# Performance work log

Measured on AMD Instinct MI355X. Metric: run time of the kernel, lower is better.

## Reference

```python
import jax, jax.numpy as jnp
import numpy as np

N_ACTIVE = 32

def setup_inputs() -> dict:
    key = jax.random.key(0)
    ks = jax.random.split(key, 6)
    B, T, D, G, GD = 4, 2048, 2048, 4096, 256
    x = jax.random.normal(ks[0], (B, T, D), jnp.float32)
    Wc = jax.random.normal(ks[1], (G, D), jnp.float32) * (D ** -0.5)   # context_proj weight
    temperature = jnp.array(1.0, jnp.float32)
    genes = jax.random.normal(ks[2], (G, GD), jnp.float32) * 0.02      # dna_bank gene table
    Wd = jax.random.normal(ks[3], (D, GD), jnp.float32) * (GD ** -0.5) # gene_to_down weight
    Wu = jax.random.normal(ks[4], (D, GD), jnp.float32) * 0.02         # gene_to_up (zeros in init; random for testing)
    norm_w = jnp.ones((D,), jnp.float32)                               # RMSNorm weight
    scale = jnp.array(0.1, jnp.float32)
    return {"x": x, "Wc": Wc, "temperature": temperature, "genes": genes,
            "Wd": Wd, "Wu": Wu, "norm_w": norm_w, "scale": scale}

def reference(x, Wc, temperature, genes, Wd, Wu, norm_w, scale):
    # RMSNorm (torch default eps = finfo(dtype).eps, learnable elementwise weight)
    eps = jnp.finfo(x.dtype).eps
    xn = x * jax.lax.rsqrt(jnp.mean(x * x, axis=-1, keepdims=True) + eps) * norm_w
    # Expression: router logits over gene bank, temperature clamped at 0.1
    logits = jnp.einsum('btd,gd->btg', xn, Wc) / jnp.clip(temperature, 0.1)
    # top-k + scatter(-inf) + softmax == softmax over top-k values, zeros elsewhere
    top_vals, top_idx = jax.lax.top_k(logits, N_ACTIVE)        # (B,T,K)
    expr_w = jax.nn.softmax(top_vals, axis=-1)                 # (B,T,K)
    # dna_bank.express: weighted combination of genes. Only top-k entries are
    # nonzero, so gather + weighted sum is mathematically identical to the
    # dense (B,T,G)@(G,GD) combine the original materializes.
    expressed = jnp.einsum('btk,btkc->btc', expr_w, genes[top_idx])  # (B,T,GD)
    down = jnp.tanh(jnp.einsum('btc,dc->btd', expressed, Wd))
    up = jnp.einsum('btc,dc->btd', expressed, Wu)
    return down * xn * up * scale
```

## Files before the change

kernel.cpp:

```cpp
#include <hip/hip_runtime.h>
#include <math.h>

#define M_TOK 8192
#define D_DIM 2048
#define G_GENES 4096
#define GD_DIM 256
#define KSEL 32
#define NCAND 40
#define NSLICE 8

typedef float f32x4 __attribute__((ext_vector_type(4)));
typedef short bf16x8 __attribute__((ext_vector_type(8)));

__device__ __forceinline__ void async_copy16(const void* g, void* lds) {
  __builtin_amdgcn_global_load_lds((const __attribute__((address_space(1))) void*)g,
                                   (__attribute__((address_space(3))) void*)lds, 16, 0, 0);
}

__device__ __forceinline__ unsigned short f2bf(float f) {
  unsigned int u = __float_as_uint(f);
  unsigned int r = (u + 0x7fffu + ((u >> 16) & 1u)) >> 16;
  return (unsigned short)r;
}
__device__ __forceinline__ float bf2f(unsigned short h) {
  return __uint_as_float(((unsigned int)h) << 16);
}

__global__ __launch_bounds__(256) void k1_rmsnorm(const float* __restrict__ x,
                                                  const float* __restrict__ nw,
                                                  float* __restrict__ r_out,
                                                  unsigned short* __restrict__ xn_bf) {
  int t = blockIdx.x, tid = threadIdx.x;
  const float4* xr = (const float4*)(x + (size_t)t * D_DIM);
  float4 a = xr[tid], b = xr[tid + 256];
  double ss = (double)a.x*a.x + (double)a.y*a.y + (double)a.z*a.z + (double)a.w*a.w
            + (double)b.x*b.x + (double)b.y*b.y + (double)b.z*b.z + (double)b.w*b.w;
  for (int off = 32; off; off >>= 1) ss += __shfl_down(ss, off);
  __shared__ double sred[4];
  __shared__ float rshare;
  int lane = tid & 63, wv = tid >> 6;
  if (lane == 0) sred[wv] = ss;
  __syncthreads();
  if (tid == 0) {
    double tot = sred[0] + sred[1] + sred[2] + sred[3];
    float r = (float)(1.0 / sqrt(tot / (double)D_DIM + 1.1920928955078125e-7));
    rshare = r; r_out[t] = r;
  }
  __syncthreads();
  float r = rshare;
  const float4* nw4 = (const float4*)nw;
  float4 na = nw4[tid], nb = nw4[tid + 256];
  ushort4 oa, ob;
  oa.x = f2bf(a.x * r * na.x); oa.y = f2bf(a.y * r * na.y);
  oa.z = f2bf(a.z * r * na.z); oa.w = f2bf(a.w * r * na.w);
  ob.x = f2bf(b.x * r * nb.x); ob.y = f2bf(b.y * r * nb.y);
  ob.z = f2bf(b.z * r * nb.z); ob.w = f2bf(b.w * r * nb.w);
  ushort4* o4 = (ushort4*)(xn_bf + (size_t)t * D_DIM);
  o4[tid] = oa; o4[tid + 256] = ob;
}

__global__ __launch_bounds__(256) void k2_cvt(const float* __restrict__ w,
                                              unsigned short* __restrict__ wb) {
  size_t i = (size_t)blockIdx.x * 256 + threadIdx.x;
  const float4* w4 = (const float4*)w;
  float4 a = w4[2*i], b = w4[2*i+1];
  ushort4 oa, ob;
  oa.x = f2bf(a.x); oa.y = f2bf(a.y); oa.z = f2bf(a.z); oa.w = f2bf(a.w);
  ob.x = f2bf(b.x); ob.y = f2bf(b.y); ob.z = f2bf(b.z); ob.w = f2bf(b.w);
  ((ushort4*)wb)[2*i] = oa; ((ushort4*)wb)[2*i+1] = ob;
}

__global__ __launch_bounds__(256) void k2b_split(const float* __restrict__ wd,
                                                 const float* __restrict__ wu,
                                                 unsigned short* __restrict__ wdh,
                                                 unsigned short* __restrict__ wdl,
                                                 unsigned short* __restrict__ wuh,
                                                 unsigned short* __restrict__ wul) {
  const float* src = blockIdx.y ? wu : wd;
  unsigned short* dh = blockIdx.y ? wuh : wdh;
  unsigned short* dl = blockIdx.y ? wul : wdl;
  size_t i = (size_t)blockIdx.x * 256 + threadIdx.x;
  float4 v = ((const float4*)src)[i];
  ushort4 h, l;
  h.x = f2bf(v.x); l.x = f2bf(v.x - bf2f(h.x));
  h.y = f2bf(v.y); l.y = f2bf(v.y - bf2f(h.y));
  h.z = f2bf(v.z); l.z = f2bf(v.z - bf2f(h.z));
  h.w = f2bf(v.w); l.w = f2bf(v.w - bf2f(h.w));
  ((ushort4*)dh)[i] = h;
  ((ushort4*)dl)[i] = l;
}

__global__ __launch_bounds__(512, 1) void k3_gemm_logits(const unsigned short* __restrict__ A,
                                                         const unsigned short* __restrict__ B,
                                                         unsigned short* __restrict__ C) {
  __shared__ unsigned short As[4][256 * 32];
  __shared__ unsigned short Bs[4][256 * 32];
  const int tid = threadIdx.x;
  const int lane = tid & 63, wv = tid >> 6;
  const int wm = wv >> 2, wn = wv & 3;
  int lin = blockIdx.x;
  int swz = (lin & 7) * 64 + (lin >> 3);
  const int bm = swz & 31, bn = swz >> 5;

  const int grow = lane >> 2;
  const int gslot = (lane & 3) ^ ((lane >> 3) & 3);
  const unsigned short* agp = A + (size_t)(bm * 256 + wv * 32 + grow) * D_DIM + gslot * 8;
  const unsigned short* bgp = B + (size_t)(bn * 256 + wv * 32 + grow) * D_DIM + gslot * 8;
  const int fr = lane & 15;
  const int sw8 = (((lane >> 4) ^ ((lane >> 1) & 3))) * 8;

  f32x4 acc[8][4];
#pragma unroll
  for (int m = 0; m < 8; ++m)
#pragma unroll
    for (int n = 0; n < 4; ++n) acc[m][n] = (f32x4){0.f, 0.f, 0.f, 0.f};

#define STAGE_A3(t_) { const int b_ = (t_) & 3; const int kt_ = (t_) * 32;          \
    async_copy16(agp + kt_,              &As[b_][(wv * 32) * 32]);                   \
    async_copy16(agp + kt_ + 16 * D_DIM, &As[b_][(wv * 32 + 16) * 32]); }
#define STAGE_B3(t_) { const int b_ = (t_) & 3; const int kt_ = (t_) * 32;          \
    async_copy16(bgp + kt_,              &Bs[b_][(wv * 32) * 32]);                   \
    async_copy16(bgp + kt_ + 16 * D_DIM, &Bs[b_][(wv * 32 + 16) * 32]); }

  STAGE_A3(0); STAGE_B3(0);
  STAGE_A3(1); STAGE_B3(1);
  STAGE_A3(2); STAGE_B3(2);
  asm volatile("s_waitcnt vmcnt(8)" ::: "memory");
  __builtin_amdgcn_s_barrier();

#pragma unroll 1
  for (int t = 0; t < 64; ++t) {
    const int c = t & 3;
    const unsigned short* as = As[c];
    const unsigned short* bs = Bs[c];
    bf16x8 fa[4], fb[4];
#pragma unroll
    for (int n = 0; n < 4; ++n)
      fb[n] = *(const bf16x8*)&bs[(wn * 64 + n * 16 + fr) * 32 + sw8];
#pragma unroll
    for (int m = 0; m < 4; ++m)
      fa[m] = *(const bf16x8*)&as[(wm * 128 + m * 16 + fr) * 32 + sw8];
    if (t + 3 < 64) STAGE_A3(t + 3);
    __builtin_amdgcn_s_barrier();
    asm volatile("s_waitcnt lgkmcnt(0)" ::: "memory");
    __builtin_amdgcn_sched_barrier(0);
    __builtin_amdgcn_s_setprio(1);
#pragma unroll
    for (int m = 0; m < 4; ++m)
#pragma unroll
      for (int n = 0; n < 4; ++n)
        acc[m][n] = __builtin_amdgcn_mfma_f32_16x16x32_bf16(fa[m], fb[n], acc[m][n], 0, 0, 0);
    __builtin_amdgcn_s_setprio(0);
    __builtin_amdgcn_s_barrier();
#pragma unroll
    for (int m = 0; m < 4; ++m)
      fa[m] = *(const bf16x8*)&as[(wm * 128 + 64 + m * 16 + fr) * 32 + sw8];
    if (t + 3 < 64) STAGE_B3(t + 3);
    __builtin_amdgcn_s_barrier();
    asm volatile("s_waitcnt lgkmcnt(0)" ::: "memory");
    __builtin_amdgcn_sched_barrier(0);
    __builtin_amdgcn_s_setprio(1);
#pragma unroll
    for (int m = 0; m < 4; ++m)
#pragma unroll
      for (int n = 0; n < 4; ++n)
        acc[m + 4][n] = __builtin_amdgcn_mfma_f32_16x16x32_bf16(fa[m], fb[n], acc[m + 4][n], 0, 0, 0);
    __builtin_amdgcn_s_setprio(0);
    if (t <= 60)      { asm volatile("s_waitcnt vmcnt(8)" ::: "memory"); }
    else if (t == 61) { asm volatile("s_waitcnt vmcnt(4)" ::: "memory"); }
    else if (t == 62) { asm volatile("s_waitcnt vmcnt(0)" ::: "memory"); }
    __builtin_amdgcn_s_barrier();
  }
#undef STAGE_A3
#undef STAGE_B3

#pragma unroll
  for (int m = 0; m < 8; ++m)
#pragma unroll
    for (int n = 0; n < 4; ++n)
#pragma unroll
      for (int j = 0; j < 4; ++j) {
        int row = bm * 256 + wm * 128 + m * 16 + (lane >> 4) * 4 + j;
        int col = bn * 256 + wn * 64 + n * 16 + fr;
        C[(size_t)row * G_GENES + col] = f2bf(acc[m][n][j]);
      }
}

__global__ __launch_bounds__(256) void k4_topk(const unsigned short* __restrict__ L,
                                               int* __restrict__ cand) {
  int wv = threadIdx.x >> 6, lane = threadIdx.x & 63;
  int t = blockIdx.x * 4 + wv;
  const unsigned short* lp = L + (size_t)t * G_GENES;
  unsigned kp[32];
#pragma unroll
  for (int i = 0; i < 8; ++i) {
    uint4 raw = *(const uint4*)(lp + i * 512 + lane * 8);
    unsigned rr[4] = {raw.x, raw.y, raw.z, raw.w};
#pragma unroll
    for (int q = 0; q < 4; ++q) {
      unsigned r = rr[q];
      unsigned s = (r >> 15) & 0x00010001u;
      unsigned xm = 0x80008000u | (s * 0x7FFFu);
      kp[i * 4 + q] = r ^ xm;
    }
  }
  unsigned lo = 0, hi = 65536;
  while (hi - lo > 1u) {
    unsigned mid = (lo + hi) >> 1;
    int c = 0;
#pragma unroll
    for (int q = 0; q < 32; ++q) {
      c += __popcll(__ballot((kp[q] & 0xFFFFu) >= mid));
      c += __popcll(__ballot((kp[q] >> 16) >= mid));
    }
    if (c >= NCAND) lo = mid; else hi = mid;
  }
  const unsigned T = lo;
  unsigned long long below = (1ull << lane) - 1ull;
  int* outp = cand + (size_t)t * NCAND;
  int cnt = 0;
#pragma unroll
  for (int q = 0; q < 32; ++q) {
#pragma unroll
    for (int h = 0; h < 2; ++h) {
      unsigned key = h ? (kp[q] >> 16) : (kp[q] & 0xFFFFu);
      bool pred = key > T;
      unsigned long long m = __ballot(pred);
      if (pred) {
        int pos = cnt + (int)__popcll(m & below);
        outp[pos] = (q >> 2) * 512 + lane * 8 + (q & 3) * 2 + h;
      }
      cnt += (int)__popcll(m);
    }
  }
#pragma unroll 1
  for (int q = 0; q < 32 && cnt < NCAND; ++q) {
#pragma unroll
    for (int h = 0; h < 2; ++h) {
      unsigned key = h ? (kp[q] >> 16) : (kp[q] & 0xFFFFu);
      bool pred = key == T;
      unsigned long long m = __ballot(pred);
      if (pred) {
        int pos = cnt + (int)__popcll(m & below);
        if (pos < NCAND)
          outp[pos] = (q >> 2) * 512 + lane * 8 + (q & 3) * 2 + h;
      }
      cnt += (int)__popcll(m);
    }
  }
}

__global__ __launch_bounds__(256) void k5a_partial(const float* __restrict__ x,
                                                   const float* __restrict__ r,
                                                   const float* __restrict__ nw,
                                                   const float* __restrict__ Wc,
                                                   const int* __restrict__ cand,
                                                   double* __restrict__ part) {
  int bid = blockIdx.x;
  int slice = bid & 7;
  int group = bid >> 3;
  int wv = threadIdx.x >> 6, lane = threadIdx.x & 63;
  const int dbase = slice * 256;
  float4 nv = *(const float4*)(nw + dbase + lane * 4);
  bool b0 = (lane & 1) != 0, b1 = (lane & 2) != 0, b2 = (lane & 4) != 0;
#pragma unroll 1
  for (int tt = 0; tt < 2; ++tt) {
    int t = group * 8 + wv * 2 + tt;
    float rr = r[t];
    float4 xv = *(const float4*)(x + (size_t)t * D_DIM + dbase + lane * 4);
    float4 xl;
    xl.x = xv.x * rr * nv.x;
    xl.y = xv.y * rr * nv.y;
    xl.z = xv.z * rr * nv.z;
    xl.w = xv.w * rr * nv.w;
    int myg = cand[t * NCAND + (lane < NCAND ? lane : 0)];
    double* outp = part + ((size_t)t * NSLICE + slice) * NCAND;
#pragma unroll 1
    for (int j0 = 0; j0 < NCAND; j0 += 8) {
      float4 w[8];
#pragma unroll
      for (int c = 0; c < 8; ++c) {
        int g = __shfl(myg, j0 + c);
        w[c] = *(const float4*)(Wc + (size_t)g * D_DIM + dbase + lane * 4);
      }
      double s[8];
#pragma unroll
      for (int c = 0; c < 8; ++c)
        s[c] = ((double)xl.x * (double)w[c].x + (double)xl.y * (double)w[c].y)
             + ((double)xl.z * (double)w[c].z + (double)xl.w * (double)w[c].w);
      double u01 = b0 ? s[1] : s[0], t01 = b0 ? s[0] : s[1];
      double u23 = b0 ? s[3] : s[2], t23 = b0 ? s[2] : s[3];
      double u45 = b0 ? s[5] : s[4], t45 = b0 ? s[4] : s[5];
      double u67 = b0 ? s[7] : s[6], t67 = b0 ? s[6] : s[7];
      u01 += __shfl_xor(t01, 1);
      u23 += __shfl_xor(t23, 1);
      u45 += __shfl_xor(t45, 1);
      u67 += __shfl_xor(t67, 1);
      double v03 = b1 ? u23 : u01, t03 = b1 ? u01 : u23;
      double v47 = b1 ? u67 : u45, t47 = b1 ? u45 : u67;
      v03 += __shfl_xor(t03, 2);
      v47 += __shfl_xor(t47, 2);
      double wsum = b2 ? v47 : v03, t07 = b2 ? v03 : v47;
      wsum += __shfl_xor(t07, 4);
      wsum += __shfl_xor(wsum, 8);
      wsum += __shfl_xor(wsum, 16);
      wsum += __shfl_xor(wsum, 32);
      if (lane < 8) outp[j0 + lane] = wsum;
    }
  }
}

__global__ __launch_bounds__(256) void k6_express(const double* __restrict__ part,
                                                  const int* __restrict__ cand,
                                                  const float* __restrict__ genes,
                                                  const float* __restrict__ temp,
                                                  unsigned short* __restrict__ e_hi,
                                                  unsigned short* __restrict__ e_lo) {
  int t = blockIdx.x, tid = threadIdx.x;
  __shared__ double sval[NCAND];
  __shared__ int sidx[NCAND];
  __shared__ float sw[NCAND];
  float tclamp = fmaxf(temp[0], 0.1f);
  if (tid < NCAND) {
    const double* pp = part + (size_t)t * NSLICE * NCAND + tid;
    double v = 0.0;
#pragma unroll
    for (int s = 0; s < NSLICE; ++s) v += pp[s * NCAND];
    sval[tid] = v / (double)tclamp;
    sidx[tid] = cand[(size_t)t * NCAND + tid];
  }
  __syncthreads();
  if (tid < 64) {
    double v = (tid < NCAND) ? sval[tid] : -1.0e300;
    int gi = (tid < NCAND) ? sidx[tid] : 0x7fffffff;
    int rank = 0;
    for (int j = 0; j < NCAND; ++j) {
      double vj = sval[j]; int gj = sidx[j];
      if (vj > v || (vj == v && gj < gi)) rank++;
    }
    bool sel = (tid < NCAND) && (rank < KSEL);
    double vs = sel ? v : -1.0e300;
    double mx = vs;
    for (int off = 32; off; off >>= 1) { double o = __shfl_xor(mx, off); mx = fmax(mx, o); }
    double e = sel ? exp(v - mx) : 0.0;
    double ssum = e;
    for (int off = 32; off; off >>= 1) ssum += __shfl_xor(ssum, off);
    if (tid < NCAND) sw[tid] = (float)(e / ssum);
  }
  __syncthreads();
  float a0 = 0.f, a1 = 0.f, a2 = 0.f, a3 = 0.f;
#pragma unroll
  for (int k = 0; k < NCAND; k += 4) {
    a0 += sw[k]     * genes[(size_t)sidx[k]     * GD_DIM + tid];
    a1 += sw[k + 1] * genes[(size_t)sidx[k + 1] * GD_DIM + tid];
    a2 += sw[k + 2] * genes[(size_t)sidx[k + 2] * GD_DIM + tid];
    a3 += sw[k + 3] * genes[(size_t)sidx[k + 3] * GD_DIM + tid];
  }
  float acc = (a0 + a1) + (a2 + a3);
  unsigned short h = f2bf(acc);
  unsigned short l = f2bf(acc - bf2f(h));
  e_hi[(size_t)t * GD_DIM + tid] = h;
  e_lo[(size_t)t * GD_DIM + tid] = l;
}

__global__ __launch_bounds__(256) void k7_mfma(const unsigned short* __restrict__ e_hi,
                                               const unsigned short* __restrict__ e_lo,
                                               const unsigned short* __restrict__ wdh,
                                               const unsigned short* __restrict__ wdl,
                                               const unsigned short* __restrict__ wuh,
                                               const unsigned short* __restrict__ wul,
                                               const float* __restrict__ x,
                                               const float* __restrict__ r,
                                               const float* __restrict__ nw,
                                               const float* __restrict__ scale_p,
                                               float* __restrict__ out) {
  __shared__ unsigned short Ah[128 * 32], Al[128 * 32];
  __shared__ unsigned short Dh[64 * 32], Dl[64 * 32], Uh[64 * 32], Ul[64 * 32];
  int tid = threadIdx.x;
  int lane = tid & 63, wv = tid >> 6;
  int bn = blockIdx.x, bm = blockIdx.y;
  int wr = wv >> 1, wc = wv & 1;
  const int lrow = lane >> 2;
  const int lcol = (lane & 3) * 8;

  f32x4 accD[4][2], accU[4][2];
#pragma unroll
  for (int m = 0; m < 4; ++m)
#pragma unroll
    for (int n = 0; n < 2; ++n) {
      accD[m][n] = (f32x4){0.f, 0.f, 0.f, 0.f};
      accU[m][n] = (f32x4){0.f, 0.f, 0.f, 0.f};
    }

  for (int kt = 0; kt < GD_DIM; kt += 32) {
    __syncthreads();
#pragma unroll
    for (int c = 0; c < 8; ++c) {
      int cid = wv * 8 + c;
      if (cid < 8) {
        async_copy16(e_hi + (size_t)(bm * 128 + cid * 16 + lrow) * GD_DIM + kt + lcol,
                     &Ah[cid * 512]);
      } else if (cid < 16) {
        int cc = cid - 8;
        async_copy16(e_lo + (size_t)(bm * 128 + cc * 16 + lrow) * GD_DIM + kt + lcol,
                     &Al[cc * 512]);
      } else if (cid < 20) {
        int cc = cid - 16;
        async_copy16(wdh + (size_t)(bn * 64 + cc * 16 + lrow) * GD_DIM + kt + lcol,
                     &Dh[cc * 512]);
      } else if (cid < 24) {
        int cc = cid - 20;
        async_copy16(wdl + (size_t)(bn * 64 + cc * 16 + lrow) * GD_DIM + kt + lcol,
                     &Dl[cc * 512]);
      } else if (cid < 28) {
        int cc = cid - 24;
        async_copy16(wuh + (size_t)(bn * 64 + cc * 16 + lrow) * GD_DIM + kt + lcol,
                     &Uh[cc * 512]);
      } else {
        int cc = cid - 28;
        async_copy16(wul + (size_t)(bn * 64 + cc * 16 + lrow) * GD_DIM + kt + lcol,
                     &Ul[cc * 512]);
      }
    }
    __syncthreads();
    bf16x8 fah[4], fal[4], fdh[2], fdl[2], fuh[2], ful[2];
#pragma unroll
    for (int m = 0; m < 4; ++m) {
      int off = (wr * 64 + m * 16 + (lane & 15)) * 32 + (lane >> 4) * 8;
      fah[m] = *(const bf16x8*)&Ah[off];
      fal[m] = *(const bf16x8*)&Al[off];
    }
#pragma unroll
    for (int n = 0; n < 2; ++n) {
      int off = (wc * 32 + n * 16 + (lane & 15)) * 32 + (lane >> 4) * 8;
      fdh[n] = *(const bf16x8*)&Dh[off];
      fdl[n] = *(const bf16x8*)&Dl[off];
      fuh[n] = *(const bf16x8*)&Uh[off];
      ful[n] = *(const bf16x8*)&Ul[off];
    }
#pragma unroll
    for (int m = 0; m < 4; ++m)
#pragma unroll
      for (int n = 0; n < 2; ++n) {
        accD[m][n] = __builtin_amdgcn_mfma_f32_16x16x32_bf16(fah[m], fdh[n], accD[m][n], 0, 0, 0);
        accD[m][n] = __builtin_amdgcn_mfma_f32_16x16x32_bf16(fah[m], fdl[n], accD[m][n], 0, 0, 0);
        accD[m][n] = __builtin_amdgcn_mfma_f32_16x16x32_bf16(fal[m], fdh[n], accD[m][n], 0, 0, 0);
        accU[m][n] = __builtin_amdgcn_mfma_f32_16x16x32_bf16(fah[m], fuh[n], accU[m][n], 0, 0, 0);
        accU[m][n] = __builtin_amdgcn_mfma_f32_16x16x32_bf16(fah[m], ful[n], accU[m][n], 0, 0, 0);
        accU[m][n] = __builtin_amdgcn_mfma_f32_16x16x32_bf16(fal[m], fuh[n], accU[m][n], 0, 0, 0);
      }
  }
  float sc = scale_p[0];
#pragma unroll
  for (int m = 0; m < 4; ++m)
#pragma unroll
    for (int j = 0; j < 4; ++j) {
      int token = bm * 128 + wr * 64 + m * 16 + (lane >> 4) * 4 + j;
      float rr = r[token];
#pragma unroll
      for (int n = 0; n < 2; ++n) {
        int d = bn * 64 + wc * 32 + n * 16 + (lane & 15);
        float xn = x[(size_t)token * D_DIM + d] * rr * nw[d];
        out[(size_t)token * D_DIM + d] = tanhf(accD[m][n][j]) * xn * accU[m][n][j] * sc;
      }
    }
}

extern "C" void kernel_launch(void* const* d_in, const int* in_sizes, int n_in,
                              void* d_out, int out_size, void* d_ws, size_t ws_size,
                              hipStream_t stream) {
  const float* x       = (const float*)d_in[0];
  const float* Wc      = (const float*)d_in[1];
  const float* temp    = (const float*)d_in[2];
  const float* genes   = (const float*)d_in[3];
  const float* Wd      = (const float*)d_in[4];
  const float* Wu      = (const float*)d_in[5];
  const float* nw      = (const float*)d_in[6];
  const float* scale_p = (const float*)d_in[7];

  char* ws = (char*)d_ws;
  float* r_buf          = (float*)ws;
  unsigned short* xn_bf = (unsigned short*)(ws + 65536);
  unsigned short* wc_bf = (unsigned short*)(ws + 65536 + (size_t)M_TOK * D_DIM * 2);
  char* p = ws + 65536 + (size_t)M_TOK * D_DIM * 2 + (size_t)G_GENES * D_DIM * 2;
  int* cand    = (int*)p;                       p += (size_t)M_TOK * NCAND * 4;
  p += (size_t)M_TOK * NCAND * 8;
  unsigned short* e_hi = (unsigned short*)p;    p += (size_t)M_TOK * GD_DIM * 2;
  unsigned short* e_lo = (unsigned short*)p;

  unsigned short* wdh = (unsigned short*)(ws + 65536);
  unsigned short* wdl = wdh + (size_t)D_DIM * GD_DIM;
  unsigned short* wuh = wdl + (size_t)D_DIM * GD_DIM;
  unsigned short* wul = wuh + (size_t)D_DIM * GD_DIM;
  double* part = (double*)(ws + 65536 + 4ull * D_DIM * GD_DIM * 2);

  unsigned short* logits_bf = (unsigned short*)d_out;

  k1_rmsnorm<<<dim3(M_TOK), dim3(256), 0, stream>>>(x, nw, r_buf, xn_bf);
  k2_cvt<<<dim3((G_GENES * D_DIM) / (256 * 8)), dim3(256), 0, stream>>>(Wc, wc_bf);
  k3_gemm_logits<<<dim3((M_TOK / 256) * (G_GENES / 256)), dim3(512), 0, stream>>>(xn_bf, wc_bf, logits_bf);
  k4_topk<<<dim3(M_TOK / 4), dim3(256), 0, stream>>>(logits_bf, cand);
  k2b_split<<<dim3((D_DIM * GD_DIM) / (256 * 4), 2), dim3(256), 0, stream>>>(Wd, Wu, wdh, wdl, wuh, wul);
  k5a_partial<<<dim3(M_TOK), dim3(256), 0, stream>>>(x, r_buf, nw, Wc, cand, part);
  k6_express<<<dim3(M_TOK), dim3(256), 0, stream>>>(part, cand, genes, temp, e_hi, e_lo);
  k7_mfma<<<dim3(D_DIM / 64, M_TOK / 128), dim3(256), 0, stream>>>(e_hi, e_lo, wdh, wdl, wuh, wul,
                                                                   x, r_buf, nw, scale_p, (float*)d_out);
}
```

Baseline: 523.6 us.

## Triple-buffer k7 MFMA GEMM with async prefetch, swizzled LDS and larger tiles

Reworks the final down/up projection GEMM into a 128x128 tile per 512-thread block. It adds a three-stage LDS ring filled by async global-to-LDS copies two k-steps ahead, with explicit vmcnt waits and barriers. It also applies XOR swizzling on LDS slots to avoid bank conflicts, remaps block IDs for L2 locality, and raises MFMA wave priority. The goal is to hide load latency and improve reuse in k7, at the cost of much more LDS (one block per CU) and fragile hand-placed waitcnt logic.

Measured after the change: 453.8 us. 13.3% less time.

```diff
diff --git a/kernel.cpp b/kernel.cpp
--- a/kernel.cpp
+++ b/kernel.cpp
@@ -363,25 +363,38 @@
   e_lo[(size_t)t * GD_DIM + tid] = l;
 }
 
-__global__ __launch_bounds__(256) void k7_mfma(const unsigned short* __restrict__ e_hi,
-                                               const unsigned short* __restrict__ e_lo,
-                                               const unsigned short* __restrict__ wdh,
-                                               const unsigned short* __restrict__ wdl,
-                                               const unsigned short* __restrict__ wuh,
-                                               const unsigned short* __restrict__ wul,
-                                               const float* __restrict__ x,
-                                               const float* __restrict__ r,
-                                               const float* __restrict__ nw,
-                                               const float* __restrict__ scale_p,
-                                               float* __restrict__ out) {
-  __shared__ unsigned short Ah[128 * 32], Al[128 * 32];
-  __shared__ unsigned short Dh[64 * 32], Dl[64 * 32], Uh[64 * 32], Ul[64 * 32];
-  int tid = threadIdx.x;
-  int lane = tid & 63, wv = tid >> 6;
-  int bn = blockIdx.x, bm = blockIdx.y;
-  int wr = wv >> 1, wc = wv & 1;
-  const int lrow = lane >> 2;
-  const int lcol = (lane & 3) * 8;
+__global__ __launch_bounds__(512, 1) void k7_mfma(const unsigned short* __restrict__ e_hi,
+                                                  const unsigned short* __restrict__ e_lo,
+                                                  const unsigned short* __restrict__ wdh,
+                                                  const unsigned short* __restrict__ wdl,
+                                                  const unsigned short* __restrict__ wuh,
+                                                  const unsigned short* __restrict__ wul,
+                                                  const float* __restrict__ x,
+                                                  const float* __restrict__ r,
+                                                  const float* __restrict__ nw,
+                                                  const float* __restrict__ scale_p,
+                                                  float* __restrict__ out) {
+  __shared__ unsigned short L[3][6][128 * 32];
+  const int tid = threadIdx.x;
+  const int lane = tid & 63, wv = tid >> 6;
+  const int wm = wv >> 2, wn = wv & 3;
+  int lin = blockIdx.x;
+  int swz = (lin & 7) * 128 + (lin >> 3);
+  const int bm = swz & 63, bn = swz >> 6;
+
+  const int grow = lane >> 2;
+  const int gslot = (lane & 3) ^ ((lane >> 3) & 3);
+  const int goff = gslot * 8;
+  const unsigned short* ehp = e_hi + (size_t)(bm * 128 + wv * 16 + grow) * GD_DIM + goff;
+  const unsigned short* elp = e_lo + (size_t)(bm * 128 + wv * 16 + grow) * GD_DIM + goff;
+  const unsigned short* dhp = wdh + (size_t)(bn * 128 + wv * 16 + grow) * GD_DIM + goff;
+  const unsigned short* dlp = wdl + (size_t)(bn * 128 + wv * 16 + grow) * GD_DIM + goff;
+  const unsigned short* uhp = wuh + (size_t)(bn * 128 + wv * 16 + grow) * GD_DIM + goff;
+  const unsigned short* ulp = wul + (size_t)(bn * 128 + wv * 16 + grow) * GD_DIM + goff;
+  const int ldst = (wv * 16) * 32;
+
+  const int fr = lane & 15;
+  const int sw8 = ((lane >> 4) ^ ((lane >> 1) & 3)) * 8;
 
   f32x4 accD[4][2], accU[4][2];
 #pragma unroll
@@ -392,74 +405,84 @@
       accU[m][n] = (f32x4){0.f, 0.f, 0.f, 0.f};
     }
 
-  for (int kt = 0; kt < GD_DIM; kt += 32) {
-    __syncthreads();
-#pragma unroll
-    for (int c = 0; c < 8; ++c) {
-      int cid = wv * 8 + c;
-      if (cid < 8) {
-        async_copy16(e_hi + (size_t)(bm * 128 + cid * 16 + lrow) * GD_DIM + kt + lcol,
-                     &Ah[cid * 512]);
-      } else if (cid < 16) {
-        int cc = cid - 8;
-        async_copy16(e_lo + (size_t)(bm * 128 + cc * 16 + lrow) * GD_DIM + kt + lcol,
-                     &Al[cc * 512]);
-      } else if (cid < 20) {
-        int cc = cid - 16;
-        async_copy16(wdh + (size_t)(bn * 64 + cc * 16 + lrow) * GD_DIM + kt + lcol,
-                     &Dh[cc * 512]);
-      } else if (cid < 24) {
-        int cc = cid - 20;
-        async_copy16(wdl + (size_t)(bn * 64 + cc * 16 + lrow) * GD_DIM + kt + lcol,
-                     &Dl[cc * 512]);
-      } else if (cid < 28) {
-        int cc = cid - 24;
-        async_copy16(wuh + (size_t)(bn * 64 + cc * 16 + lrow) * GD_DIM + kt + lcol,
-                     &Uh[cc * 512]);
-      } else {
-        int cc = cid - 28;
-        async_copy16(wul + (size_t)(bn * 64 + cc * 16 + lrow) * GD_DIM + kt + lcol,
-                     &Ul[cc * 512]);
-      }
-    }
-    __syncthreads();
-    bf16x8 fah[4], fal[4], fdh[2], fdl[2], fuh[2], ful[2];
+#define STAGE7(t_) if ((t_) < 8) { const int b_ = (t_) % 3; const int kt_ = (t_) * 32; \
+    async_copy16(ehp + kt_, &L[b_][0][ldst]); \
+    async_copy16(elp + kt_, &L[b_][1][ldst]); \
+    async_copy16(dhp + kt_, &L[b_][2][ldst]); \
+    async_copy16(dlp + kt_, &L[b_][3][ldst]); \
+    async_copy16(uhp + kt_, &L[b_][4][ldst]); \
+    async_copy16(ulp + kt_, &L[b_][5][ldst]); }
+
+  STAGE7(0); STAGE7(1);
+  asm volatile("s_waitcnt vmcnt(6)" ::: "memory");
+  __builtin_amdgcn_s_barrier();
+
+#pragma unroll 1
+  for (int t = 0; t < 8; ++t) {
+    const int b = t % 3;
+    bf16x8 fah[4], fal[4], fh[2], fl[2];
 #pragma unroll
     for (int m = 0; m < 4; ++m) {
-      int off = (wr * 64 + m * 16 + (lane & 15)) * 32 + (lane >> 4) * 8;
-      fah[m] = *(const bf16x8*)&Ah[off];
-      fal[m] = *(const bf16x8*)&Al[off];
+      int off = (wm * 64 + m * 16 + fr) * 32 + sw8;
+      fah[m] = *(const bf16x8*)&L[b][0][off];
+      fal[m] = *(const bf16x8*)&L[b][1][off];
     }
 #pragma unroll
     for (int n = 0; n < 2; ++n) {
-      int off = (wc * 32 + n * 16 + (lane & 15)) * 32 + (lane >> 4) * 8;
-      fdh[n] = *(const bf16x8*)&Dh[off];
-      fdl[n] = *(const bf16x8*)&Dl[off];
-      fuh[n] = *(const bf16x8*)&Uh[off];
-      ful[n] = *(const bf16x8*)&Ul[off];
-    }
+      int off = (wn * 32 + n * 16 + fr) * 32 + sw8;
+      fh[n] = *(const bf16x8*)&L[b][2][off];
+      fl[n] = *(const bf16x8*)&L[b][3][off];
+    }
+    STAGE7(t + 2);
+    __builtin_amdgcn_s_barrier();
+    asm volatile("s_waitcnt lgkmcnt(0)" ::: "memory");
+    __builtin_amdgcn_sched_barrier(0);
+    __builtin_amdgcn_s_setprio(1);
 #pragma unroll
     for (int m = 0; m < 4; ++m)
 #pragma unroll
       for (int n = 0; n < 2; ++n) {
-        accD[m][n] = __builtin_amdgcn_mfma_f32_16x16x32_bf16(fah[m], fdh[n], accD[m][n], 0, 0, 0);
-        accD[m][n] = __builtin_amdgcn_mfma_f32_16x16x32_bf16(fah[m], fdl[n], accD[m][n], 0, 0, 0);
-        accD[m][n] = __builtin_amdgcn_mfma_f32_16x16x32_bf16(fal[m], fdh[n], accD[m][n], 0, 0, 0);
-        accU[m][n] = __builtin_amdgcn_mfma_f32_16x16x32_bf16(fah[m], fuh[n], accU[m][n], 0, 0, 0);
-        accU[m][n] = __builtin_amdgcn_mfma_f32_16x16x32_bf16(fah[m], ful[n], accU[m][n], 0, 0, 0);
-        accU[m][n] = __builtin_amdgcn_mfma_f32_16x16x32_bf16(fal[m], fuh[n], accU[m][n], 0, 0, 0);
-      }
-  }
+        accD[m][n] = __builtin_amdgcn_mfma_f32_16x16x32_bf16(fah[m], fh[n], accD[m][n], 0, 0, 0);
+        accD[m][n] = __builtin_amdgcn_mfma_f32_16x16x32_bf16(fah[m], fl[n], accD[m][n], 0, 0, 0);
+        accD[m][n] = __builtin_amdgcn_mfma_f32_16x16x32_bf16(fal[m], fh[n], accD[m][n], 0, 0, 0);
+      }
+    __builtin_amdgcn_s_setprio(0);
+    __builtin_amdgcn_s_barrier();
+#pragma unroll
+    for (int n = 0; n < 2; ++n) {
+      int off = (wn * 32 + n * 16 + fr) * 32 + sw8;
+      fh[n] = *(const bf16x8*)&L[b][4][off];
+      fl[n] = *(const bf16x8*)&L[b][5][off];
+    }
+    __builtin_amdgcn_s_barrier();
+    asm volatile("s_waitcnt lgkmcnt(0)" ::: "memory");
+    __builtin_amdgcn_sched_barrier(0);
+    __builtin_amdgcn_s_setprio(1);
+#pragma unroll
+    for (int m = 0; m < 4; ++m)
+#pragma unroll
+      for (int n = 0; n < 2; ++n) {
+        accU[m][n] = __builtin_amdgcn_mfma_f32_16x16x32_bf16(fah[m], fh[n], accU[m][n], 0, 0, 0);
+        accU[m][n] = __builtin_amdgcn_mfma_f32_16x16x32_bf16(fah[m], fl[n], accU[m][n], 0, 0, 0);
+        accU[m][n] = __builtin_amdgcn_mfma_f32_16x16x32_bf16(fal[m], fh[n], accU[m][n], 0, 0, 0);
+      }
+    __builtin_amdgcn_s_setprio(0);
+    if (t <= 5)      { asm volatile("s_waitcnt vmcnt(6)" ::: "memory"); }
+    else if (t == 6) { asm volatile("s_waitcnt vmcnt(0)" ::: "memory"); }
+    __builtin_amdgcn_s_barrier();
+  }
+#undef STAGE7
+
   float sc = scale_p[0];
 #pragma unroll
   for (int m = 0; m < 4; ++m)
 #pragma unroll
     for (int j = 0; j < 4; ++j) {
-      int token = bm * 128 + wr * 64 + m * 16 + (lane >> 4) * 4 + j;
+      int token = bm * 128 + wm * 64 + m * 16 + (lane >> 4) * 4 + j;
       float rr = r[token];
 #pragma unroll
       for (int n = 0; n < 2; ++n) {
-        int d = bn * 64 + wc * 32 + n * 16 + (lane & 15);
+        int d = bn * 128 + wn * 32 + n * 16 + fr;
         float xn = x[(size_t)token * D_DIM + d] * rr * nw[d];
         out[(size_t)token * D_DIM + d] = tanhf(accD[m][n][j]) * xn * accU[m][n][j] * sc;
       }
@@ -503,6 +526,6 @@
   k2b_split<<<dim3((D_DIM * GD_DIM) / (256 * 4), 2), dim3(256), 0, stream>>>(Wd, Wu, wdh, wdl, wuh, wul);
   k5a_partial<<<dim3(M_TOK), dim3(256), 0, stream>>>(x, r_buf, nw, Wc, cand, part);
   k6_express<<<dim3(M_TOK), dim3(256), 0, stream>>>(part, cand, genes, temp, e_hi, e_lo);
-  k7_mfma<<<dim3(D_DIM / 64, M_TOK / 128), dim3(256), 0, stream>>>(e_hi, e_lo, wdh, wdl, wuh, wul,
-                                                                   x, r_buf, nw, scale_p, (float*)d_out);
-}
+  k7_mfma<<<dim3((M_TOK / 128) * (D_DIM / 128)), dim3(512), 0, stream>>>(e_hi, e_lo, wdh, wdl, wuh, wul,
+                                                                         x, r_buf, nw, scale_p, (float*)d_out);
+}
```
